# Kernel tuning notes

Measured on AMD Instinct MI355X. Metric: run time of the kernel, lower is better.

The kernel has to match this reference:

```python
import jax, jax.numpy as jnp
import numpy as np

B, C, OUT, H, W, M1, M2, HID = 4, 64, 64, 256, 256, 32, 32, 64
COORD = C + 1  # MLP input: channels + 1 coordinate


def _lin(key, fan_in, fan_out):
    lim = 1.0 / np.sqrt(fan_in)
    kw, kb = jax.random.split(key)
    Wm = jax.random.uniform(kw, (fan_in, fan_out), minval=-lim, maxval=lim, dtype=jnp.float32)
    b = jax.random.uniform(kb, (fan_out,), minval=-lim, maxval=lim, dtype=jnp.float32)
    return Wm, b


def setup_inputs() -> dict:
    key = jax.random.key(0)
    ks = jax.random.split(key, 12)
    x = jax.random.normal(ks[0], (B, C, H, W), dtype=jnp.float32)
    # basis_w MLP: (C+1) -> HID -> HID -> 2*M2
    wW0, wb0 = _lin(ks[1], COORD, HID)
    wW1, wb1 = _lin(ks[2], HID, HID)
    wW2, wb2 = _lin(ks[3], HID, 2 * M2)
    # basis_h MLP: (C+1) -> HID -> HID -> 2*M1
    hW0, hb0 = _lin(ks[4], COORD, HID)
    hW1, hb1 = _lin(ks[5], HID, HID)
    hW2, hb2 = _lin(ks[6], HID, 2 * M1)
    std = (1.0 / (C + OUT)) ** 0.5
    Wf_re = std * jax.random.normal(ks[7], (C, OUT, M1, M2), dtype=jnp.float32)
    Wf_im = std * jax.random.normal(ks[8], (C, OUT, M1, M2), dtype=jnp.float32)
    mixer_w, mixer_b = _lin(ks[9], OUT, OUT)
    mixer_w = mixer_w.T  # (out, in) conv1x1 layout
    sc_w, sc_b = _lin(ks[10], C, OUT)
    sc_w = sc_w.T
    return {
        "x": x,
        "wW0": wW0, "wb0": wb0, "wW1": wW1, "wb1": wb1, "wW2": wW2, "wb2": wb2,
        "hW0": hW0, "hb0": hb0, "hW1": hW1, "hb1": hb1, "hW2": hW2, "hb2": hb2,
        "Wf_re": Wf_re, "Wf_im": Wf_im,
        "mixer_w": mixer_w, "mixer_b": mixer_b,
        "sc_w": sc_w, "sc_b": sc_b,
    }


def _gelu(v):
    return jax.nn.gelu(v, approximate=False)  # torch GELU is exact erf


def _cmlp(x, W0, b0, W1, b1, W2, b2, m):
    h = _gelu(x @ W0 + b0)
    h = _gelu(h @ W1 + b1)
    o = h @ W2 + b2
    return jax.lax.complex(o[..., :m], o[..., m:])


def reference(x, wW0, wb0, wW1, wb1, wW2, wb2,
              hW0, hb0, hW1, hb1, hW2, hb2,
              Wf_re, Wf_im, mixer_w, mixer_b, sc_w, sc_b):
    Bb, Cc, Hh, Ww = x.shape
    # --- W-direction basis: input is (values, w-coord) per pixel ---
    wc = jnp.linspace(-1.0, 1.0, Ww, dtype=jnp.float32)
    w_in = jnp.concatenate(
        [jnp.transpose(x, (0, 2, 3, 1)),
         jnp.broadcast_to(wc[None, None, :, None], (Bb, Hh, Ww, 1))], axis=-1)
    wb = _cmlp(w_in, wW0, wb0, wW1, wb1, wW2, wb2, M2)  # (B,H,W,m2) complex
    xc = x.astype(jnp.complex64)
    # separable transform along W: contract W against runtime basis
    tfw = jnp.einsum('bchw,bhwm->bchm', xc, wb)  # (B,C,H,m2)
    # --- H-direction basis: input is real part of W-transform + h-coord ---
    hcv = jnp.linspace(-1.0, 1.0, Hh, dtype=jnp.float32)
    h_in = jnp.concatenate(
        [jnp.transpose(tfw.real, (0, 3, 2, 1)),
         jnp.broadcast_to(hcv[None, None, :, None], (Bb, M2, Hh, 1))], axis=-1)
    hb = _cmlp(h_in, hW0, hb0, hW1, hb1, hW2, hb2, M1)  # (B,m2,H,m1) complex
    tfhw = jnp.einsum('bchm,bmhk->bckm', tfw, hb)  # (B,C,m1,m2)
    Wf = jax.lax.complex(Wf_re, Wf_im)  # (C_in, C_out, m1, m2)
    proc = jnp.einsum('bixy,oixy->boxy', tfhw, Wf)  # (B,out,m1,m2)
    # inverse transforms with conjugate-transposed bases
    rec = jnp.einsum('bokm,bmhk->bohm', proc, jnp.conj(hb))  # (B,out,H,m2)
    spatial = jnp.einsum('bohm,bhwm->bohw', rec, jnp.conj(wb)).real / (Hh * Ww)
    y = jnp.einsum('bchw,oc->bohw', spatial, mixer_w) + mixer_b[None, :, None, None]
    y = _gelu(y)
    y = y + jnp.einsum('bchw,oc->bohw', x, sc_w) + sc_b[None, :, None, None]
    return _gelu(y)
```

## Files before the change

kernel.cpp:

```cpp
#include <hip/hip_runtime.h>
#include <math.h>


typedef __attribute__((ext_vector_type(8))) short bf16x8;
typedef __attribute__((ext_vector_type(4))) float f32x4;

__device__ __forceinline__ float gelu_f(float v) {
    const float u = v * 0.70710678118654752440f;
    const float xa = fabsf(u);
    const float t = __builtin_amdgcn_rcpf(fmaf(0.3275911f, xa, 1.0f));
    float p = fmaf(1.061405429f, t, -1.453152027f);
    p = fmaf(p, t, 1.421413741f);
    p = fmaf(p, t, -0.284496736f);
    p = fmaf(p, t, 0.254829592f);
    p *= t;
    const float e = __expf(-xa * xa);
    float erfv = fmaf(-p, e, 1.0f);
    erfv = (u < 0.0f) ? -erfv : erfv;
    return 0.5f * v * (1.0f + erfv);
}

__device__ __forceinline__ unsigned short f2b(float f) {
    union { float f; unsigned int u; } v; v.f = f;
    unsigned int u = v.u + 0x7FFFu + ((v.u >> 16) & 1u);
    return (unsigned short)(u >> 16);
}
__device__ __forceinline__ float b2f(unsigned short b) {
    union { unsigned int u; float f; } v; v.u = ((unsigned int)b) << 16;
    return v.f;
}

constexpr int MLD = 104;
constexpr int XLD = 72;

__device__ __forceinline__ ushort4 butterfly_xT(const float4 v, int q) {
    const float bx = __shfl_xor(v.x, 1);
    const float by = __shfl_xor(v.y, 1);
    const float bz = __shfl_xor(v.z, 1);
    const float bw = __shfl_xor(v.w, 1);
    float4 s1;
    s1.x = ((q & 1) == 0) ? v.x : by;
    s1.y = ((q & 1) == 0) ? bx  : v.y;
    s1.z = ((q & 1) == 0) ? v.z : bw;
    s1.w = ((q & 1) == 0) ? bz  : v.w;
    const float cx = __shfl_xor(s1.x, 2);
    const float cy = __shfl_xor(s1.y, 2);
    const float cz = __shfl_xor(s1.z, 2);
    const float cw = __shfl_xor(s1.w, 2);
    float4 s2;
    s2.x = ((q & 2) == 0) ? s1.x : cz;
    s2.y = ((q & 2) == 0) ? s1.y : cw;
    s2.z = ((q & 2) == 0) ? cx   : s1.z;
    s2.w = ((q & 2) == 0) ? cy   : s1.w;
    ushort4 u;
    u.x = f2b(s2.x); u.y = f2b(s2.y); u.z = f2b(s2.z); u.w = f2b(s2.w);
    return u;
}

__device__ __forceinline__ void stage_xT(const float* __restrict__ x,
    unsigned short* __restrict__ sA, int b, int h, int w0, int t, int LD)
{
    const int lane = t & 63, wv = t >> 6;
    const int q = lane & 3, wg = lane >> 2;
#pragma unroll
    for (int r = 0; r < 4; ++r) {
        const int cb = (r * 4 + wv) * 4;
        const float4 v = *(const float4*)&x[((size_t)(b * 64 + cb + q) * 256 + h) * 256 + w0 + wg * 4];
        const ushort4 u = butterfly_xT(v, q);
        *(ushort4*)&sA[(wg * 4 + q) * LD + cb] = u;
    }
}

__global__ void k_prep(const float* __restrict__ wW0, const float* __restrict__ wW1,
                       const float* __restrict__ wW2,
                       const float* __restrict__ hW0, const float* __restrict__ hW1,
                       const float* __restrict__ hW2,
                       unsigned short* __restrict__ wT0, unsigned short* __restrict__ wT1,
                       unsigned short* __restrict__ wT2,
                       unsigned short* __restrict__ hT0, unsigned short* __restrict__ hT1,
                       unsigned short* __restrict__ hT2)
{
    const int t = threadIdx.x;
    for (int idx = t; idx < 64 * 96; idx += 256) {
        const int o = idx / 96, k = idx % 96;
        wT0[idx] = (k < 65) ? f2b(wW0[k * 64 + o]) : (unsigned short)0;
        hT0[idx] = (k < 65) ? f2b(hW0[k * 64 + o]) : (unsigned short)0;
    }
    for (int idx = t; idx < 4096; idx += 256) {
        const int o = idx >> 6, k = idx & 63;
        wT1[idx] = f2b(wW1[k * 64 + o]);
        wT2[idx] = f2b(wW2[k * 64 + o]);
        hT1[idx] = f2b(hW1[k * 64 + o]);
        hT2[idx] = f2b(hW2[k * 64 + o]);
    }
}

__global__ __launch_bounds__(256) void k_psum(const float* __restrict__ src,
                                              float* __restrict__ dst,
                                              int nparts, int part_stride)
{
    const int i = (blockIdx.x * 256 + threadIdx.x) * 4;
    float4 acc = *(const float4*)&src[i];
    for (int p = 1; p < nparts; ++p) {
        const float4 v = *(const float4*)&src[(size_t)p * part_stride + i];
        acc.x += v.x; acc.y += v.y; acc.z += v.z; acc.w += v.w;
    }
    *(float4*)&dst[i] = acc;
}

__global__ __launch_bounds__(256) void k_psum_procT(const float* __restrict__ src,
                                                    float* __restrict__ dst)
{
    const int idx = blockIdx.x * 256 + threadIdx.x;
    const int o = idx & 63, k = (idx >> 6) & 31, m = (idx >> 11) & 31, b = idx >> 16;
    const size_t in = (size_t)(b * 64 + o) * 1024 + k * 32 + m;
    const float re = src[in] + src[524288 + in];
    const float im = src[262144 + in] + src[524288 + 262144 + in];
    dst[idx] = re;
    dst[262144 + idx] = im;
}

template<bool GELU, int NKC>
__device__ __forceinline__ void mfma_layer(
    const unsigned short* __restrict__ sW,
    const unsigned short* __restrict__ sAct,
    unsigned short* __restrict__ dst,
    const float* __restrict__ bias, int lane, int wv)
{
    const int arow = lane & 15;
    const int koff = (lane >> 4) * 8;
    const int crow = 16 * wv + (lane >> 4) * 4;
    const f32x4 zero = {0.f, 0.f, 0.f, 0.f};
    f32x4 acc[4] = {zero, zero, zero, zero};
#pragma unroll
    for (int kc = 0; kc < NKC; ++kc) {
        const bf16x8 a = *(const bf16x8*)&sW[(16 * wv + arow) * MLD + kc * 32 + koff];
#pragma unroll
        for (int nt = 0; nt < 4; ++nt) {
            const bf16x8 b = *(const bf16x8*)&sAct[(nt * 16 + arow) * MLD + kc * 32 + koff];
            acc[nt] = __builtin_amdgcn_mfma_f32_16x16x32_bf16(a, b, acc[nt], 0, 0, 0);
        }
    }
    const float4 bv = *(const float4*)&bias[crow];
#pragma unroll
    for (int nt = 0; nt < 4; ++nt) {
        const int px = nt * 16 + arow;
        float v0 = acc[nt][0] + bv.x;
        float v1 = acc[nt][1] + bv.y;
        float v2 = acc[nt][2] + bv.z;
        float v3 = acc[nt][3] + bv.w;
        if (GELU) { v0 = gelu_f(v0); v1 = gelu_f(v1); v2 = gelu_f(v2); v3 = gelu_f(v3); }
        ushort4 u;
        u.x = f2b(v0); u.y = f2b(v1); u.z = f2b(v2); u.w = f2b(v3);
        *(ushort4*)&dst[px * MLD + crow] = u;
    }
}

__device__ __forceinline__ void stage_wT96(const unsigned short* __restrict__ src,
                                           unsigned short* __restrict__ sW, int t) {
#pragma unroll
    for (int r = 0; r < 3; ++r) {
        const int idx = r * 256 + t;
        const int row = idx / 12, f = idx % 12;
        *(uint4*)&sW[row * MLD + f * 8] = *(const uint4*)&src[row * 96 + f * 8];
    }
}
__device__ __forceinline__ void stage_wT64(const unsigned short* __restrict__ src,
                                           unsigned short* __restrict__ sW, int t) {
#pragma unroll
    for (int r = 0; r < 2; ++r) {
        const int idx = r * 256 + t;
        const int row = idx >> 3, f = idx & 7;
        *(uint4*)&sW[row * MLD + f * 8] = *(const uint4*)&src[row * 64 + f * 8];
    }
}

template<bool GELU, int NKC>
__device__ __forceinline__ void mfma_layer_s(
    const unsigned short* __restrict__ sW,
    const unsigned short* __restrict__ sAct,
    unsigned short* __restrict__ dst,
    const float* __restrict__ bias, int lane, int wv)
{
    const int arow = lane & 15;
    const int g = lane >> 4;
    const int crow = 16 * wv + g * 4;
    const int sx7 = arow & 7, sx3 = arow & 3;
    const f32x4 zero = {0.f, 0.f, 0.f, 0.f};
    f32x4 acc[4] = {zero, zero, zero, zero};
#pragma unroll
    for (int kc = 0; kc < NKC; ++kc) {
        const int chraw = kc * 4 + g;
        const int ch = (chraw < 8) ? (chraw ^ sx7) : (8 + ((chraw - 8) ^ sx3));
        const bf16x8 a = *(const bf16x8*)&sW[(16 * wv + arow) * 96 + ch * 8];
#pragma unroll
        for (int nt = 0; nt < 4; ++nt) {
            const bf16x8 b = *(const bf16x8*)&sAct[(nt * 16 + arow) * 96 + ch * 8];
            acc[nt] = __builtin_amdgcn_mfma_f32_16x16x32_bf16(a, b, acc[nt], 0, 0, 0);
        }
    }
    const float4 bv = *(const float4*)&bias[crow];
    const int chw = (crow >> 3) ^ sx7;
#pragma unroll
    for (int nt = 0; nt < 4; ++nt) {
        const int px = nt * 16 + arow;
        float v0 = acc[nt][0] + bv.x;
        float v1 = acc[nt][1] + bv.y;
        float v2 = acc[nt][2] + bv.z;
        float v3 = acc[nt][3] + bv.w;
        if (GELU) { v0 = gelu_f(v0); v1 = gelu_f(v1); v2 = gelu_f(v2); v3 = gelu_f(v3); }
        ushort4 u;
        u.x = f2b(v0); u.y = f2b(v1); u.z = f2b(v2); u.w = f2b(v3);
        *(ushort4*)&dst[px * 96 + chw * 8 + (crow & 7)] = u;
    }
}

__device__ __forceinline__ void stage_wT96_s(const unsigned short* __restrict__ src,
                                             unsigned short* __restrict__ sW, int t) {
#pragma unroll
    for (int r = 0; r < 3; ++r) {
        const int idx = r * 256 + t;
        const int row = idx / 12, f = idx % 12;
        const int ch = (f < 8) ? (f ^ (row & 7)) : (8 + ((f - 8) ^ (row & 3)));
        *(uint4*)&sW[row * 96 + ch * 8] = *(const uint4*)&src[row * 96 + f * 8];
    }
}
__device__ __forceinline__ void stage_wT64_s(const unsigned short* __restrict__ src,
                                             unsigned short* __restrict__ sW, int t) {
#pragma unroll
    for (int r = 0; r < 2; ++r) {
        const int idx = r * 256 + t;
        const int row = idx >> 3, f = idx & 7;
        *(uint4*)&sW[row * 96 + ((f ^ (row & 7)) << 3)] = *(const uint4*)&src[row * 64 + f * 8];
    }
}

__global__ __launch_bounds__(256) void k_wbtfw(
    const float* __restrict__ x,
    const unsigned short* __restrict__ wT0, const float* __restrict__ b0,
    const unsigned short* __restrict__ wT1, const float* __restrict__ b1,
    const unsigned short* __restrict__ wT2, const float* __restrict__ b2,
    unsigned short* __restrict__ wb_bf, float* __restrict__ tfwM)
{
    __shared__ __align__(16) unsigned short smem[26624];
    unsigned short* sA   = smem;
    unsigned short* sB   = smem + 6144;
    unsigned short* sW   = smem + 12288;
    unsigned short* sXt  = smem + 18432;
    unsigned short* sWBt = smem + 22528;

    const int bh = blockIdx.x;
    const int b = bh >> 8, h = bh & 255;
    const int t = threadIdx.x;
    const int lane = t & 63, wv = t >> 6;
    const int arow = lane & 15, g = lane >> 4;
    const int crow = 16 * wv + g * 4;
    const int sx7 = arow & 7;
    const f32x4 zero = {0.f, 0.f, 0.f, 0.f};

    f32x4 atf[4] = {zero, zero, zero, zero};

    for (int wq = 0; wq < 4; ++wq) {
        const int w0 = wq * 64;
        __syncthreads();
        {
            const int q = lane & 3, wg = lane >> 2;
#pragma unroll
            for (int r = 0; r < 4; ++r) {
                const int cb = 16 * r + 4 * wv;
                const int c = cb + q;
                const float4 v = *(const float4*)&x[((size_t)(b * 64 + c) * 256 + h) * 256 + w0 + wg * 4];
                ushort4 ux;
                ux.x = f2b(v.x); ux.y = f2b(v.y); ux.z = f2b(v.z); ux.w = f2b(v.w);
                const int chx = (wg >> 1) ^ (c & 7);
                *(ushort4*)&sXt[c * 64 + chx * 8 + 4 * (wg & 1)] = ux;
                const ushort4 u = butterfly_xT(v, q);
                const int row = wg * 4 + q;
                const int cha = (cb >> 3) ^ (row & 7);
                *(ushort4*)&sA[row * 96 + cha * 8 + (cb & 7)] = u;
            }
        }
        if (t < 64) {
            const uint4 z = {0, 0, 0, 0};
#pragma unroll
            for (int j = 0; j < 4; ++j)
                *(uint4*)&sA[t * 96 + (8 + (j ^ (t & 3))) * 8] = z;
            sA[t * 96 + (8 + (t & 3)) * 8] = f2b((float)(w0 + t) * (2.0f / 255.0f) - 1.0f);
        }
        stage_wT96_s(wT0, sW, t);
        __syncthreads();
        mfma_layer_s<true, 3>(sW, sA, sB, b0, lane, wv);
        __syncthreads();
        stage_wT64_s(wT1, sW, t);
        __syncthreads();
        mfma_layer_s<true, 2>(sW, sB, sA, b1, lane, wv);
        __syncthreads();
        stage_wT64_s(wT2, sW, t);
        __syncthreads();
        {
            f32x4 acc[4] = {zero, zero, zero, zero};
#pragma unroll
            for (int kc = 0; kc < 2; ++kc) {
                const int ch = (kc * 4 + g) ^ sx7;
                const bf16x8 a = *(const bf16x8*)&sW[(16 * wv + arow) * 96 + ch * 8];
#pragma unroll
                for (int nt = 0; nt < 4; ++nt) {
                    const bf16x8 bb = *(const bf16x8*)&sA[(nt * 16 + arow) * 96 + ch * 8];
                    acc[nt] = __builtin_amdgcn_mfma_f32_16x16x32_bf16(a, bb, acc[nt], 0, 0, 0);
                }
            }
            const float4 bv = *(const float4*)&b2[crow];
            const int chw = (crow >> 3) ^ sx7;
#pragma unroll
            for (int nt = 0; nt < 4; ++nt) {
                const int px = nt * 16 + arow;
                ushort4 u;
                u.x = f2b(acc[nt][0] + bv.x);
                u.y = f2b(acc[nt][1] + bv.y);
                u.z = f2b(acc[nt][2] + bv.z);
                u.w = f2b(acc[nt][3] + bv.w);
                *(ushort4*)&sB[px * 96 + chw * 8 + (crow & 7)] = u;
                const int ph = px >> 3, pl = px & 7;
                sWBt[(crow + 0) * 64 + ((ph ^ ((crow + 0) & 7)) << 3) + pl] = u.x;
                sWBt[(crow + 1) * 64 + ((ph ^ ((crow + 1) & 7)) << 3) + pl] = u.y;
                sWBt[(crow + 2) * 64 + ((ph ^ ((crow + 2) & 7)) << 3) + pl] = u.z;
                sWBt[(crow + 3) * 64 + ((ph ^ ((crow + 3) & 7)) << 3) + pl] = u.w;
            }
        }
        __syncthreads();
        const size_t pixbase = (size_t)(b * 256 + h) * 256 + w0;
#pragma unroll
        for (int r = 0; r < 2; ++r) {
            const int idx = r * 256 + t;
            const int px = idx >> 3, f = idx & 7;
            *(uint4*)&wb_bf[(pixbase + px) * 64 + f * 8] =
                *(const uint4*)&sB[px * 96 + ((f ^ (px & 7)) << 3)];
        }
#pragma unroll
        for (int kc = 0; kc < 2; ++kc) {
            const int ch = (kc * 4 + g) ^ sx7;
            const bf16x8 a = *(const bf16x8*)&sWBt[(16 * wv + arow) * 64 + ch * 8];
#pragma unroll
            for (int nt = 0; nt < 4; ++nt) {
                const bf16x8 bb = *(const bf16x8*)&sXt[(nt * 16 + arow) * 64 + ch * 8];
                atf[nt] = __builtin_amdgcn_mfma_f32_16x16x32_bf16(a, bb, atf[nt], 0, 0, 0);
            }
        }
    }

    __syncthreads();
    float* sF = (float*)smem;
#pragma unroll
    for (int nt = 0; nt < 4; ++nt) {
        const int c = nt * 16 + arow;
#pragma unroll
        for (int j = 0; j < 4; ++j)
            sF[(crow + j) * 68 + c] = atf[nt][j];
    }
    __syncthreads();
#pragma unroll
    for (int r = 0; r < 4; ++r) {
        const int idx = r * 256 + t;
        const int m = idx >> 5, gg = idx & 31;
        float4 v;
        v.x = sF[m * 68 + gg * 2];
        v.y = sF[(m + 32) * 68 + gg * 2];
        v.z = sF[m * 68 + gg * 2 + 1];
        v.w = sF[(m + 32) * 68 + gg * 2 + 1];
        *(float4*)&tfwM[((size_t)(b * 32 + m) * 256 + h) * 128 + gg * 4] = v;
    }
}

__global__ __launch_bounds__(256) void k_hb_mlp2(
    const float* __restrict__ tfwM,
    const unsigned short* __restrict__ hT0, const float* __restrict__ b0,
    const unsigned short* __restrict__ hT1, const float* __restrict__ b1,
    const unsigned short* __restrict__ hT2, const float* __restrict__ b2,
    unsigned short* __restrict__ hb_bf)
{
    __shared__ __align__(16) unsigned short sA[64 * MLD];
    __shared__ __align__(16) unsigned short sB[64 * MLD];
    __shared__ __align__(16) unsigned short sW[65 * MLD];
    const int blk = blockIdx.x;
    const int bm = blk >> 2, hq = blk & 3;
    const int h0 = hq * 64;
    const int t = threadIdx.x;
    const int lane = t & 63, wv = t >> 6;

#pragma unroll
    for (int r = 0; r < 4; ++r) {
        const int idx = r * 256 + t;
        const int p = idx >> 4, f = idx & 15;
        const float* src = &tfwM[(size_t)(bm * 256 + h0 + p) * 128 + f * 8];
        const float4 u0 = *(const float4*)&src[0];
        const float4 u1 = *(const float4*)&src[4];
        ushort4 u;
        u.x = f2b(u0.x); u.y = f2b(u0.z); u.z = f2b(u1.x); u.w = f2b(u1.z);
        *(ushort4*)&sA[p * MLD + f * 4] = u;
    }
    if (t < 64) {
        const uint4 z = {0, 0, 0, 0};
        *(uint4*)&sA[t * MLD + 64] = z;
        *(uint4*)&sA[t * MLD + 72] = z;
        *(uint4*)&sA[t * MLD + 80] = z;
        *(uint4*)&sA[t * MLD + 88] = z;
        sA[t * MLD + 64] = f2b((float)(h0 + t) * (2.0f / 255.0f) - 1.0f);
    }
    stage_wT96(hT0, sW, t);
    __syncthreads();
    mfma_layer<true, 3>(sW, sA, sB, b0, lane, wv);
    __syncthreads();
    stage_wT64(hT1, sW, t);
    __syncthreads();
    mfma_layer<true, 2>(sW, sB, sA, b1, lane, wv);
    __syncthreads();
    stage_wT64(hT2, sW, t);
    __syncthreads();
    mfma_layer<false, 2>(sW, sA, sB, b2, lane, wv);
    __syncthreads();

    const size_t pixbase = (size_t)bm * 256 + h0;
#pragma unroll
    for (int r = 0; r < 2; ++r) {
        const int idx = r * 256 + t;
        const int px = idx >> 3, f = idx & 7;
        *(uint4*)&hb_bf[(pixbase + px) * 64 + f * 8] = *(const uint4*)&sB[px * MLD + f * 8];
    }
}

__global__ __launch_bounds__(256) void k_tfhw3(
    const float* __restrict__ tfwM,
    const unsigned short* __restrict__ hb_bf,
    float* __restrict__ tfhw_p)
{
    __shared__ float hr[64 * 32];
    __shared__ float hi2[64 * 32];
    __shared__ float slab[32 * 64];
    const int blk = blockIdx.x;
    const int bm = blk >> 3, chalf = (blk >> 2) & 1, hq = blk & 3;
    const int b = bm >> 5, m = bm & 31;
    const int t = threadIdx.x;
#pragma unroll
    for (int r = 0; r < 2; ++r) {
        const int q = r * 256 + t;
        const int hl = q >> 3, f = q & 7;
        const uint4 raw = *(const uint4*)&hb_bf[((size_t)bm * 256 + hq * 64 + hl) * 64 + f * 8];
        const unsigned short* us = (const unsigned short*)&raw;
        float v[8];
#pragma unroll
        for (int j = 0; j < 8; ++j) v[j] = b2f(us[j]);
        float* dst = (f < 4) ? &hr[hl * 32 + f * 8] : &hi2[hl * 32 + (f - 4) * 8];
        float4 lo; lo.x = v[0]; lo.y = v[1]; lo.z = v[2]; lo.w = v[3];
        float4 hi; hi.x = v[4]; hi.y = v[5]; hi.z = v[6]; hi.w = v[7];
        *(float4*)&dst[0] = lo;
        *(float4*)&dst[4] = hi;
    }
    const int k = t & 31, cq = t >> 5;
    float accr[4] = {0.f, 0.f, 0.f, 0.f}, acci[4] = {0.f, 0.f, 0.f, 0.f};
    const size_t tbase = (size_t)bm * 32768;
    for (int ht = 0; ht < 2; ++ht) {
        __syncthreads();
#pragma unroll
        for (int r = 0; r < 2; ++r) {
            const int q = r * 256 + t;
            const int hl = q >> 3, f = q & 7;
            *(float4*)&slab[hl * 64 + f * 4] =
                *(const float4*)&tfwM[tbase + (size_t)(hq * 64 + ht * 32 + hl) * 128 + chalf * 64 + f * 4];
        }
        __syncthreads();
#pragma unroll 8
        for (int hl = 0; hl < 32; ++hl) {
            const float hrv = hr[(ht * 32 + hl) * 32 + k];
            const float hiv = hi2[(ht * 32 + hl) * 32 + k];
            const float4 u0 = *(const float4*)&slab[hl * 64 + cq * 8];
            const float4 u1 = *(const float4*)&slab[hl * 64 + cq * 8 + 4];
            accr[0] = fmaf(u0.x, hrv, fmaf(-u0.y, hiv, accr[0]));
            acci[0] = fmaf(u0.x, hiv, fmaf( u0.y, hrv, acci[0]));
            accr[1] = fmaf(u0.z, hrv, fmaf(-u0.w, hiv, accr[1]));
            acci[1] = fmaf(u0.z, hiv, fmaf( u0.w, hrv, acci[1]));
            accr[2] = fmaf(u1.x, hrv, fmaf(-u1.y, hiv, accr[2]));
            acci[2] = fmaf(u1.x, hiv, fmaf( u1.y, hrv, acci[2]));
            accr[3] = fmaf(u1.z, hrv, fmaf(-u1.w, hiv, accr[3]));
            acci[3] = fmaf(u1.z, hiv, fmaf( u1.w, hrv, acci[3]));
        }
    }
    float* tp = tfhw_p + (size_t)hq * 524288;
#pragma unroll
    for (int i = 0; i < 4; ++i) {
        const int c = chalf * 32 + cq * 4 + i;
        const size_t po = ((size_t)(b * 64 + c) * 32 + k) * 32 + m;
        tp[po] = accr[i];
        tp[262144 + po] = acci[i];
    }
}

__global__ __launch_bounds__(256) void k_proc2(
    const float* __restrict__ tfhw,
    const float* __restrict__ Wf_re, const float* __restrict__ Wf_im,
    float* __restrict__ proc_p)
{
    const int blk = blockIdx.x;
    const int o = blk >> 3, kq = (blk >> 1) & 3, chalf = blk & 1;
    const int t = threadIdx.x;
    const int mo = kq * 256 + t;
    const float* tre = tfhw;
    const float* tim = tfhw + 262144;
    float accr[4] = {0.f, 0.f, 0.f, 0.f}, acci[4] = {0.f, 0.f, 0.f, 0.f};
    for (int cc = 0; cc < 32; ++cc) {
        const int c = chalf * 32 + cc;
        const float wfr = Wf_re[(size_t)(c * 64 + o) * 1024 + mo];
        const float wfi = Wf_im[(size_t)(c * 64 + o) * 1024 + mo];
#pragma unroll
        for (int bb = 0; bb < 4; ++bb) {
            const float tr = tre[(size_t)(bb * 64 + c) * 1024 + mo];
            const float ti = tim[(size_t)(bb * 64 + c) * 1024 + mo];
            accr[bb] = fmaf(tr, wfr, fmaf(-ti, wfi, accr[bb]));
            acci[bb] = fmaf(tr, wfi, fmaf(ti, wfr, acci[bb]));
        }
    }
    float* pp = proc_p + (size_t)chalf * 524288;
#pragma unroll
    for (int bb = 0; bb < 4; ++bb) {
        pp[(size_t)(bb * 64 + o) * 1024 + mo] = accr[bb];
        pp[262144 + (size_t)(bb * 64 + o) * 1024 + mo] = acci[bb];
    }
}

__global__ __launch_bounds__(256) void k_rec4(
    const float* __restrict__ procT,
    const unsigned short* __restrict__ hb_bf,
    unsigned short* __restrict__ recO)
{
    __shared__ float lhr[32 * 32];
    __shared__ float lhi[32 * 32];
    const int blk = blockIdx.x;
    const int bm = blk >> 3, hq = blk & 7;
    const int b = bm >> 5, m = bm & 31;
    const int t = threadIdx.x;
    {
        const int hl = t >> 3, f = t & 7;
        const uint4 raw = *(const uint4*)&hb_bf[((size_t)bm * 256 + hq * 32 + hl) * 64 + f * 8];
        const unsigned short* us = (const unsigned short*)&raw;
        float v[8];
#pragma unroll
        for (int j = 0; j < 8; ++j) v[j] = b2f(us[j]);
        float* dst = (f < 4) ? &lhr[hl * 32 + f * 8] : &lhi[hl * 32 + (f - 4) * 8];
        float4 lo; lo.x = v[0]; lo.y = v[1]; lo.z = v[2]; lo.w = v[3];
        float4 hi; hi.x = v[4]; hi.y = v[5]; hi.z = v[6]; hi.w = v[7];
        *(float4*)&dst[0] = lo;
        *(float4*)&dst[4] = hi;
    }
    const int o = t & 63, hg = t >> 6;
    const float* pr = procT + (size_t)(b * 32 + m) * 2048 + o;
    const float* pi = pr + 262144;
    float Pr[32], Pi[32];
#pragma unroll
    for (int k = 0; k < 32; ++k) {
        Pr[k] = pr[k * 64];
        Pi[k] = pi[k * 64];
    }
    __syncthreads();
    for (int hh = 0; hh < 8; ++hh) {
        const int hl = hg * 8 + hh;
        float ar = 0.f, ai = 0.f;
#pragma unroll
        for (int k4 = 0; k4 < 8; ++k4) {
            const float4 hr4 = *(const float4*)&lhr[hl * 32 + k4 * 4];
            const float4 hi4 = *(const float4*)&lhi[hl * 32 + k4 * 4];
            ar = fmaf(Pr[k4*4+0], hr4.x, fmaf(Pi[k4*4+0], hi4.x, ar));
            ai = fmaf(Pi[k4*4+0], hr4.x, fmaf(-Pr[k4*4+0], hi4.x, ai));
            ar = fmaf(Pr[k4*4+1], hr4.y, fmaf(Pi[k4*4+1], hi4.y, ar));
            ai = fmaf(Pi[k4*4+1], hr4.y, fmaf(-Pr[k4*4+1], hi4.y, ai));
            ar = fmaf(Pr[k4*4+2], hr4.z, fmaf(Pi[k4*4+2], hi4.z, ar));
            ai = fmaf(Pi[k4*4+2], hr4.z, fmaf(-Pr[k4*4+2], hi4.z, ai));
            ar = fmaf(Pr[k4*4+3], hr4.w, fmaf(Pi[k4*4+3], hi4.w, ar));
            ai = fmaf(Pi[k4*4+3], hr4.w, fmaf(-Pr[k4*4+3], hi4.w, ai));
        }
        const int h = hq * 32 + hl;
        const size_t rb = ((size_t)(b * 256 + h) * 64 + o) * 64;
        recO[rb + m]      = f2b(ar);
        recO[rb + 32 + m] = f2b(ai);
    }
}

__global__ __launch_bounds__(256) void k_final4(
    const float* __restrict__ x,
    const unsigned short* __restrict__ wb_bf,
    const unsigned short* __restrict__ recO,
    const float* __restrict__ mw, const float* __restrict__ mb,
    const float* __restrict__ scw, const float* __restrict__ scb,
    float* __restrict__ out)
{
    constexpr int LD = 72;
    __shared__ __align__(16) unsigned short sWb[64 * LD];
    __shared__ __align__(16) unsigned short sR [64 * LD];
    __shared__ __align__(16) unsigned short sX [64 * LD];
    __shared__ __align__(16) unsigned short sS [64 * LD];
    const int blk = blockIdx.x;
    const int b = blk >> 10, h = (blk >> 2) & 255, wq = blk & 3;
    const int w0 = wq * 64;
    const int t = threadIdx.x;
    const int lane = t & 63, wv = t >> 6;
    const size_t pixbase = (size_t)(b * 256 + h) * 256 + w0;

#pragma unroll
    for (int r = 0; r < 2; ++r) {
        const int idx = r * 256 + t;
        const int px = idx >> 3, f = idx & 7;
        *(uint4*)&sWb[px * LD + f * 8] = *(const uint4*)&wb_bf[(pixbase + px) * 64 + f * 8];
    }
    const size_t recbase = (size_t)(b * 256 + h) * 4096;
#pragma unroll
    for (int r = 0; r < 2; ++r) {
        const int idx = r * 256 + t;
        const int o = idx >> 3, f = idx & 7;
        *(uint4*)&sR[o * LD + f * 8] = *(const uint4*)&recO[recbase + (size_t)o * 64 + f * 8];
    }
    stage_xT(x, sX, b, h, w0, t, LD);
    __syncthreads();

    const int arow = lane & 15;
    const int koff = (lane >> 4) * 8;
    const f32x4 zero = {0.f, 0.f, 0.f, 0.f};

    f32x4 accA[4] = {zero, zero, zero, zero};
#pragma unroll
    for (int kc = 0; kc < 2; ++kc) {
        const bf16x8 a = *(const bf16x8*)&sR[(16 * wv + arow) * LD + kc * 32 + koff];
#pragma unroll
        for (int nt = 0; nt < 4; ++nt) {
            const bf16x8 bb = *(const bf16x8*)&sWb[(nt * 16 + arow) * LD + kc * 32 + koff];
            accA[nt] = __builtin_amdgcn_mfma_f32_16x16x32_bf16(a, bb, accA[nt], 0, 0, 0);
        }
    }
    __syncthreads();

    const int crow = 16 * wv + (lane >> 4) * 4;
#pragma unroll
    for (int nt = 0; nt < 4; ++nt) {
        const int px = nt * 16 + arow;
#pragma unroll
        for (int j = 0; j < 4; ++j)
            sS[px * LD + crow + j] = f2b(accA[nt][j] * (1.0f / 65536.0f));
    }
#pragma unroll
    for (int r = 0; r < 4; ++r) {
        const int idx = r * 256 + t;
        const int o = idx >> 4, cq = idx & 15;
        const float4 v1 = *(const float4*)&mw[o * 64 + cq * 4];
        ushort4 u1;
        u1.x = f2b(v1.x); u1.y = f2b(v1.y); u1.z = f2b(v1.z); u1.w = f2b(v1.w);
        *(ushort4*)&sWb[o * LD + cq * 4] = u1;
        const float4 v2 = *(const float4*)&scw[o * 64 + cq * 4];
        ushort4 u2;
        u2.x = f2b(v2.x); u2.y = f2b(v2.y); u2.z = f2b(v2.z); u2.w = f2b(v2.w);
        *(ushort4*)&sR[o * LD + cq * 4] = u2;
    }
    __syncthreads();

    f32x4 accB[4] = {zero, zero, zero, zero};
    f32x4 accC[4] = {zero, zero, zero, zero};
#pragma unroll
    for (int kc = 0; kc < 2; ++kc) {
        const bf16x8 am = *(const bf16x8*)&sWb[(16 * wv + arow) * LD + kc * 32 + koff];
        const bf16x8 as = *(const bf16x8*)&sR [(16 * wv + arow) * LD + kc * 32 + koff];
#pragma unroll
        for (int nt = 0; nt < 4; ++nt) {
            const bf16x8 bs = *(const bf16x8*)&sS[(nt * 16 + arow) * LD + kc * 32 + koff];
            const bf16x8 bx = *(const bf16x8*)&sX[(nt * 16 + arow) * LD + kc * 32 + koff];
            accB[nt] = __builtin_amdgcn_mfma_f32_16x16x32_bf16(am, bs, accB[nt], 0, 0, 0);
            accC[nt] = __builtin_amdgcn_mfma_f32_16x16x32_bf16(as, bx, accC[nt], 0, 0, 0);
        }
    }

#pragma unroll
    for (int nt = 0; nt < 4; ++nt) {
        const int px = nt * 16 + arow;
#pragma unroll
        for (int j = 0; j < 4; ++j) {
            const int o = crow + j;
            const float y = gelu_f(accB[nt][j] + mb[o]);
            const float z = y + accC[nt][j] + scb[o];
            out[((size_t)(b * 64 + o) * 256 + h) * 256 + w0 + px] = gelu_f(z);
        }
    }
}

extern "C" void kernel_launch(void* const* d_in, const int* in_sizes, int n_in,
                              void* d_out, int out_size, void* d_ws, size_t ws_size,
                              hipStream_t stream) {
    const float* x    = (const float*)d_in[0];
    const float* wW0  = (const float*)d_in[1];
    const float* wb0  = (const float*)d_in[2];
    const float* wW1  = (const float*)d_in[3];
    const float* wb1  = (const float*)d_in[4];
    const float* wW2  = (const float*)d_in[5];
    const float* wb2  = (const float*)d_in[6];
    const float* hW0  = (const float*)d_in[7];
    const float* hb0  = (const float*)d_in[8];
    const float* hW1  = (const float*)d_in[9];
    const float* hb1  = (const float*)d_in[10];
    const float* hW2  = (const float*)d_in[11];
    const float* hb2  = (const float*)d_in[12];
    const float* Wf_re = (const float*)d_in[13];
    const float* Wf_im = (const float*)d_in[14];
    const float* mw   = (const float*)d_in[15];
    const float* mbv  = (const float*)d_in[16];
    const float* scw  = (const float*)d_in[17];
    const float* scb  = (const float*)d_in[18];

    char* base = (char*)d_ws;
    unsigned short* wb_bf = (unsigned short*)(base + 0);
    float* tfwM   = (float*)(base + 33554432);
    unsigned short* hb_bf = (unsigned short*)(base + 50331648);
    float* tfhw_p = (float*)(base + 54525952);
    float* tfhw   = (float*)(base + 62914560);
    float* proc_p = (float*)(base + 65011712);
    float* procT  = (float*)(base + 69206016);
    unsigned short* recO = (unsigned short*)(base + 71303168);
    unsigned short* wT0 = (unsigned short*)(base + 79691776);
    unsigned short* wT1 = (unsigned short*)(base + 79704064);
    unsigned short* wT2 = (unsigned short*)(base + 79712256);
    unsigned short* hT0 = (unsigned short*)(base + 79720448);
    unsigned short* hT1 = (unsigned short*)(base + 79732736);
    unsigned short* hT2 = (unsigned short*)(base + 79740928);

    k_prep<<<1, 256, 0, stream>>>(wW0, wW1, wW2, hW0, hW1, hW2,
                                  wT0, wT1, wT2, hT0, hT1, hT2);
    k_wbtfw<<<1024, 256, 0, stream>>>(x, wT0, wb0, wT1, wb1, wT2, wb2, wb_bf, tfwM);
    k_hb_mlp2<<<512, 256, 0, stream>>>(tfwM, hT0, hb0, hT1, hb1, hT2, hb2, hb_bf);
    k_tfhw3<<<1024, 256, 0, stream>>>(tfwM, hb_bf, tfhw_p);
    k_psum<<<1024, 256, 0, stream>>>(tfhw_p, tfhw, 4, 524288);
    k_proc2<<<512, 256, 0, stream>>>(tfhw, Wf_re, Wf_im, proc_p);
    k_psum_procT<<<1024, 256, 0, stream>>>(proc_p, procT);
    k_rec4<<<1024, 256, 0, stream>>>(procT, hb_bf, recO);
    k_final4<<<4096, 256, 0, stream>>>(x, wb_bf, recO, mw, mbv, scw, scb, (float*)d_out);
}
```

Before: 184.7 us.

## Hold MLP weights in registers and reuse bf16 transposed x in final kernel

The MLP weight fragments and biases are now loaded straight into registers once per block, in both the W-basis and H-basis MLP kernels. This removes the repeated shared-memory weight staging and the barriers between layers. The W-basis kernel also writes the bf16 transposed x tile it already builds to a new workspace buffer. The final kernel then loads that buffer instead of re-reading fp32 x and shuffling it into transposed form. The H-MLP moves to the swizzled 96-wide shared layout. The cost is more registers, an extra 32MB write, and a larger workspace.

```diff
diff --git a/kernel.cpp b/kernel.cpp
--- a/kernel.cpp
+++ b/kernel.cpp
@@ -29,9 +29,6 @@
     union { unsigned int u; float f; } v; v.u = ((unsigned int)b) << 16;
     return v.f;
 }
-
-constexpr int MLD = 104;
-constexpr int XLD = 72;
 
 __device__ __forceinline__ ushort4 butterfly_xT(const float4 v, int q) {
     const float bx = __shfl_xor(v.x, 1);
@@ -57,20 +54,6 @@
     return u;
 }
 
-__device__ __forceinline__ void stage_xT(const float* __restrict__ x,
-    unsigned short* __restrict__ sA, int b, int h, int w0, int t, int LD)
-{
-    const int lane = t & 63, wv = t >> 6;
-    const int q = lane & 3, wg = lane >> 2;
-#pragma unroll
-    for (int r = 0; r < 4; ++r) {
-        const int cb = (r * 4 + wv) * 4;
-        const float4 v = *(const float4*)&x[((size_t)(b * 64 + cb + q) * 256 + h) * 256 + w0 + wg * 4];
-        const ushort4 u = butterfly_xT(v, q);
-        *(ushort4*)&sA[(wg * 4 + q) * LD + cb] = u;
-    }
-}
-
 __global__ void k_prep(const float* __restrict__ wW0, const float* __restrict__ wW1,
                        const float* __restrict__ wW2,
                        const float* __restrict__ hW0, const float* __restrict__ hW1,
@@ -121,69 +104,12 @@
 }
 
 template<bool GELU, int NKC>
-__device__ __forceinline__ void mfma_layer(
-    const unsigned short* __restrict__ sW,
+__device__ __forceinline__ void mfma_layer_r(
+    const bf16x8* __restrict__ wf,
     const unsigned short* __restrict__ sAct,
     unsigned short* __restrict__ dst,
-    const float* __restrict__ bias, int lane, int wv)
-{
-    const int arow = lane & 15;
-    const int koff = (lane >> 4) * 8;
-    const int crow = 16 * wv + (lane >> 4) * 4;
-    const f32x4 zero = {0.f, 0.f, 0.f, 0.f};
-    f32x4 acc[4] = {zero, zero, zero, zero};
-#pragma unroll
-    for (int kc = 0; kc < NKC; ++kc) {
-        const bf16x8 a = *(const bf16x8*)&sW[(16 * wv + arow) * MLD + kc * 32 + koff];
-#pragma unroll
-        for (int nt = 0; nt < 4; ++nt) {
-            const bf16x8 b = *(const bf16x8*)&sAct[(nt * 16 + arow) * MLD + kc * 32 + koff];
-            acc[nt] = __builtin_amdgcn_mfma_f32_16x16x32_bf16(a, b, acc[nt], 0, 0, 0);
-        }
-    }
-    const float4 bv = *(const float4*)&bias[crow];
-#pragma unroll
-    for (int nt = 0; nt < 4; ++nt) {
-        const int px = nt * 16 + arow;
-        float v0 = acc[nt][0] + bv.x;
-        float v1 = acc[nt][1] + bv.y;
-        float v2 = acc[nt][2] + bv.z;
-        float v3 = acc[nt][3] + bv.w;
-        if (GELU) { v0 = gelu_f(v0); v1 = gelu_f(v1); v2 = gelu_f(v2); v3 = gelu_f(v3); }
-        ushort4 u;
-        u.x = f2b(v0); u.y = f2b(v1); u.z = f2b(v2); u.w = f2b(v3);
-        *(ushort4*)&dst[px * MLD + crow] = u;
-    }
-}
-
-__device__ __forceinline__ void stage_wT96(const unsigned short* __restrict__ src,
-                                           unsigned short* __restrict__ sW, int t) {
-#pragma unroll
-    for (int r = 0; r < 3; ++r) {
-        const int idx = r * 256 + t;
-        const int row = idx / 12, f = idx % 12;
-        *(uint4*)&sW[row * MLD + f * 8] = *(const uint4*)&src[row * 96 + f * 8];
-    }
-}
-__device__ __forceinline__ void stage_wT64(const unsigned short* __restrict__ src,
-                                           unsigned short* __restrict__ sW, int t) {
-#pragma unroll
-    for (int r = 0; r < 2; ++r) {
-        const int idx = r * 256 + t;
-        const int row = idx >> 3, f = idx & 7;
-        *(uint4*)&sW[row * MLD + f * 8] = *(const uint4*)&src[row * 64 + f * 8];
-    }
-}
-
-template<bool GELU, int NKC>
-__device__ __forceinline__ void mfma_layer_s(
-    const unsigned short* __restrict__ sW,
-    const unsigned short* __restrict__ sAct,
-    unsigned short* __restrict__ dst,
-    const float* __restrict__ bias, int lane, int wv)
-{
-    const int arow = lane & 15;
-    const int g = lane >> 4;
+    const float4 bv, int arow, int g, int wv)
+{
     const int crow = 16 * wv + g * 4;
     const int sx7 = arow & 7, sx3 = arow & 3;
     const f32x4 zero = {0.f, 0.f, 0.f, 0.f};
@@ -192,14 +118,12 @@
     for (int kc = 0; kc < NKC; ++kc) {
         const int chraw = kc * 4 + g;
         const int ch = (chraw < 8) ? (chraw ^ sx7) : (8 + ((chraw - 8) ^ sx3));
-        const bf16x8 a = *(const bf16x8*)&sW[(16 * wv + arow) * 96 + ch * 8];
 #pragma unroll
         for (int nt = 0; nt < 4; ++nt) {
             const bf16x8 b = *(const bf16x8*)&sAct[(nt * 16 + arow) * 96 + ch * 8];
-            acc[nt] = __builtin_amdgcn_mfma_f32_16x16x32_bf16(a, b, acc[nt], 0, 0, 0);
-        }
-    }
-    const float4 bv = *(const float4*)&bias[crow];
+            acc[nt] = __builtin_amdgcn_mfma_f32_16x16x32_bf16(wf[kc], b, acc[nt], 0, 0, 0);
+        }
+    }
     const int chw = (crow >> 3) ^ sx7;
 #pragma unroll
     for (int nt = 0; nt < 4; ++nt) {
@@ -215,39 +139,19 @@
     }
 }
 
-__device__ __forceinline__ void stage_wT96_s(const unsigned short* __restrict__ src,
-                                             unsigned short* __restrict__ sW, int t) {
-#pragma unroll
-    for (int r = 0; r < 3; ++r) {
-        const int idx = r * 256 + t;
-        const int row = idx / 12, f = idx % 12;
-        const int ch = (f < 8) ? (f ^ (row & 7)) : (8 + ((f - 8) ^ (row & 3)));
-        *(uint4*)&sW[row * 96 + ch * 8] = *(const uint4*)&src[row * 96 + f * 8];
-    }
-}
-__device__ __forceinline__ void stage_wT64_s(const unsigned short* __restrict__ src,
-                                             unsigned short* __restrict__ sW, int t) {
-#pragma unroll
-    for (int r = 0; r < 2; ++r) {
-        const int idx = r * 256 + t;
-        const int row = idx >> 3, f = idx & 7;
-        *(uint4*)&sW[row * 96 + ((f ^ (row & 7)) << 3)] = *(const uint4*)&src[row * 64 + f * 8];
-    }
-}
-
 __global__ __launch_bounds__(256) void k_wbtfw(
     const float* __restrict__ x,
     const unsigned short* __restrict__ wT0, const float* __restrict__ b0,
     const unsigned short* __restrict__ wT1, const float* __restrict__ b1,
     const unsigned short* __restrict__ wT2, const float* __restrict__ b2,
-    unsigned short* __restrict__ wb_bf, float* __restrict__ tfwM)
-{
-    __shared__ __align__(16) unsigned short smem[26624];
+    unsigned short* __restrict__ wb_bf, unsigned short* __restrict__ xT_bf,
+    float* __restrict__ tfwM)
+{
+    __shared__ __align__(16) unsigned short smem[20480];
     unsigned short* sA   = smem;
     unsigned short* sB   = smem + 6144;
-    unsigned short* sW   = smem + 12288;
-    unsigned short* sXt  = smem + 18432;
-    unsigned short* sWBt = smem + 22528;
+    unsigned short* sXt  = smem + 12288;
+    unsigned short* sWBt = smem + 16384;
 
     const int bh = blockIdx.x;
     const int b = bh >> 8, h = bh & 255;
@@ -257,6 +161,20 @@
     const int crow = 16 * wv + g * 4;
     const int sx7 = arow & 7;
     const f32x4 zero = {0.f, 0.f, 0.f, 0.f};
+
+    const int wrow = 16 * wv + arow;
+    bf16x8 w0f[3], w1f[2], w2f[2];
+#pragma unroll
+    for (int kc = 0; kc < 3; ++kc)
+        w0f[kc] = *(const bf16x8*)&wT0[wrow * 96 + (kc * 4 + g) * 8];
+#pragma unroll
+    for (int kc = 0; kc < 2; ++kc) {
+        w1f[kc] = *(const bf16x8*)&wT1[wrow * 64 + (kc * 4 + g) * 8];
+        w2f[kc] = *(const bf16x8*)&wT2[wrow * 64 + (kc * 4 + g) * 8];
+    }
+    const float4 bv0 = *(const float4*)&b0[crow];
+    const float4 bv1 = *(const float4*)&b1[crow];
+    const float4 bv2 = *(const float4*)&b2[crow];
 
     f32x4 atf[4] = {zero, zero, zero, zero};
 
@@ -287,38 +205,39 @@
                 *(uint4*)&sA[t * 96 + (8 + (j ^ (t & 3))) * 8] = z;
             sA[t * 96 + (8 + (t & 3)) * 8] = f2b((float)(w0 + t) * (2.0f / 255.0f) - 1.0f);
         }
-        stage_wT96_s(wT0, sW, t);
         __syncthreads();
-        mfma_layer_s<true, 3>(sW, sA, sB, b0, lane, wv);
+        const size_t pixbase = (size_t)(b * 256 + h) * 256 + w0;
+#pragma unroll
+        for (int r = 0; r < 2; ++r) {
+            const int idx = r * 256 + t;
+            const int px = idx >> 3, f = idx & 7;
+            *(uint4*)&xT_bf[(pixbase + px) * 64 + f * 8] =
+                *(const uint4*)&sA[px * 96 + ((f ^ (px & 7)) << 3)];
+        }
+        mfma_layer_r<true, 3>(w0f, sA, sB, bv0, arow, g, wv);
         __syncthreads();
-        stage_wT64_s(wT1, sW, t);
-        __syncthreads();
-        mfma_layer_s<true, 2>(sW, sB, sA, b1, lane, wv);
-        __syncthreads();
-        stage_wT64_s(wT2, sW, t);
+        mfma_layer_r<true, 2>(w1f, sB, sA, bv1, arow, g, wv);
         __syncthreads();
         {
             f32x4 acc[4] = {zero, zero, zero, zero};
 #pragma unroll
             for (int kc = 0; kc < 2; ++kc) {
                 const int ch = (kc * 4 + g) ^ sx7;
-                const bf16x8 a = *(const bf16x8*)&sW[(16 * wv + arow) * 96 + ch * 8];
 #pragma unroll
                 for (int nt = 0; nt < 4; ++nt) {
                     const bf16x8 bb = *(const bf16x8*)&sA[(nt * 16 + arow) * 96 + ch * 8];
-                    acc[nt] = __builtin_amdgcn_mfma_f32_16x16x32_bf16(a, bb, acc[nt], 0, 0, 0);
+                    acc[nt] = __builtin_amdgcn_mfma_f32_16x16x32_bf16(w2f[kc], bb, acc[nt], 0, 0, 0);
                 }
             }
-            const float4 bv = *(const float4*)&b2[crow];
             const int chw = (crow >> 3) ^ sx7;
 #pragma unroll
             for (int nt = 0; nt < 4; ++nt) {
                 const int px = nt * 16 + arow;
                 ushort4 u;
-                u.x = f2b(acc[nt][0] + bv.x);
-                u.y = f2b(acc[nt][1] + bv.y);
-                u.z = f2b(acc[nt][2] + bv.z);
-                u.w = f2b(acc[nt][3] + bv.w);
+                u.x = f2b(acc[nt][0] + bv2.x);
+                u.y = f2b(acc[nt][1] + bv2.y);
+                u.z = f2b(acc[nt][2] + bv2.z);
+                u.w = f2b(acc[nt][3] + bv2.w);
                 *(ushort4*)&sB[px * 96 + chw * 8 + (crow & 7)] = u;
                 const int ph = px >> 3, pl = px & 7;
                 sWBt[(crow + 0) * 64 + ((ph ^ ((crow + 0) & 7)) << 3) + pl] = u.x;
@@ -328,7 +247,6 @@
             }
         }
         __syncthreads();
-        const size_t pixbase = (size_t)(b * 256 + h) * 256 + w0;
 #pragma unroll
         for (int r = 0; r < 2; ++r) {
             const int idx = r * 256 + t;
@@ -371,21 +289,36 @@
     }
 }
 
-__global__ __launch_bounds__(256) void k_hb_mlp2(
+__global__ __launch_bounds__(256) void k_hb_mlp3(
     const float* __restrict__ tfwM,
     const unsigned short* __restrict__ hT0, const float* __restrict__ b0,
     const unsigned short* __restrict__ hT1, const float* __restrict__ b1,
     const unsigned short* __restrict__ hT2, const float* __restrict__ b2,
     unsigned short* __restrict__ hb_bf)
 {
-    __shared__ __align__(16) unsigned short sA[64 * MLD];
-    __shared__ __align__(16) unsigned short sB[64 * MLD];
-    __shared__ __align__(16) unsigned short sW[65 * MLD];
+    __shared__ __align__(16) unsigned short sA[64 * 96];
+    __shared__ __align__(16) unsigned short sB[64 * 96];
     const int blk = blockIdx.x;
     const int bm = blk >> 2, hq = blk & 3;
     const int h0 = hq * 64;
     const int t = threadIdx.x;
     const int lane = t & 63, wv = t >> 6;
+    const int arow = lane & 15, g = lane >> 4;
+    const int crow = 16 * wv + g * 4;
+
+    const int wrow = 16 * wv + arow;
+    bf16x8 h0f[3], h1f[2], h2f[2];
+#pragma unroll
+    for (int kc = 0; kc < 3; ++kc)
+        h0f[kc] = *(const bf16x8*)&hT0[wrow * 96 + (kc * 4 + g) * 8];
+#pragma unroll
+    for (int kc = 0; kc < 2; ++kc) {
+        h1f[kc] = *(const bf16x8*)&hT1[wrow * 64 + (kc * 4 + g) * 8];
+        h2f[kc] = *(const bf16x8*)&hT2[wrow * 64 + (kc * 4 + g) * 8];
+    }
+    const float4 bv0 = *(const float4*)&b0[crow];
+    const float4 bv1 = *(const float4*)&b1[crow];
+    const float4 bv2 = *(const float4*)&b2[crow];
 
 #pragma unroll
     for (int r = 0; r < 4; ++r) {
@@ -396,27 +329,22 @@
         const float4 u1 = *(const float4*)&src[4];
         ushort4 u;
         u.x = f2b(u0.x); u.y = f2b(u0.z); u.z = f2b(u1.x); u.w = f2b(u1.z);
-        *(ushort4*)&sA[p * MLD + f * 4] = u;
+        const int ch = (f >> 1) ^ (p & 7);
+        *(ushort4*)&sA[p * 96 + ch * 8 + 4 * (f & 1)] = u;
     }
     if (t < 64) {
         const uint4 z = {0, 0, 0, 0};
-        *(uint4*)&sA[t * MLD + 64] = z;
-        *(uint4*)&sA[t * MLD + 72] = z;
-        *(uint4*)&sA[t * MLD + 80] = z;
-        *(uint4*)&sA[t * MLD + 88] = z;
-        sA[t * MLD + 64] = f2b((float)(h0 + t) * (2.0f / 255.0f) - 1.0f);
-    }
-    stage_wT96(hT0, sW, t);
-    __syncthreads();
-    mfma_layer<true, 3>(sW, sA, sB, b0, lane, wv);
-    __syncthreads();
-    stage_wT64(hT1, sW, t);
-    __syncthreads();
-    mfma_layer<true, 2>(sW, sB, sA, b1, lane, wv);
-    __syncthreads();
-    stage_wT64(hT2, sW, t);
-    __syncthreads();
-    mfma_layer<false, 2>(sW, sA, sB, b2, lane, wv);
+#pragma unroll
+        for (int j = 0; j < 4; ++j)
+            *(uint4*)&sA[t * 96 + (8 + (j ^ (t & 3))) * 8] = z;
+        sA[t * 96 + (8 + (t & 3)) * 8] = f2b((float)(h0 + t) * (2.0f / 255.0f) - 1.0f);
+    }
+    __syncthreads();
+    mfma_layer_r<true, 3>(h0f, sA, sB, bv0, arow, g, wv);
+    __syncthreads();
+    mfma_layer_r<true, 2>(h1f, sB, sA, bv1, arow, g, wv);
+    __syncthreads();
+    mfma_layer_r<false, 2>(h2f, sA, sB, bv2, arow, g, wv);
     __syncthreads();
 
     const size_t pixbase = (size_t)bm * 256 + h0;
@@ -424,7 +352,8 @@
     for (int r = 0; r < 2; ++r) {
         const int idx = r * 256 + t;
         const int px = idx >> 3, f = idx & 7;
-        *(uint4*)&hb_bf[(pixbase + px) * 64 + f * 8] = *(const uint4*)&sB[px * MLD + f * 8];
+        *(uint4*)&hb_bf[(pixbase + px) * 64 + f * 8] =
+            *(const uint4*)&sB[px * 96 + ((f ^ (px & 7)) << 3)];
     }
 }
 
@@ -584,7 +513,7 @@
 }
 
 __global__ __launch_bounds__(256) void k_final4(
-    const float* __restrict__ x,
+    const unsigned short* __restrict__ xT_bf,
     const unsigned short* __restrict__ wb_bf,
     const unsigned short* __restrict__ recO,
     const float* __restrict__ mw, const float* __restrict__ mb,
@@ -616,7 +545,12 @@
         const int o = idx >> 3, f = idx & 7;
         *(uint4*)&sR[o * LD + f * 8] = *(const uint4*)&recO[recbase + (size_t)o * 64 + f * 8];
     }
-    stage_xT(x, sX, b, h, w0, t, LD);
+#pragma unroll
+    for (int r = 0; r < 2; ++r) {
+        const int idx = r * 256 + t;
+        const int px = idx >> 3, f = idx & 7;
+        *(uint4*)&sX[px * LD + f * 8] = *(const uint4*)&xT_bf[(pixbase + px) * 64 + f * 8];
+    }
     __syncthreads();
 
     const int arow = lane & 15;
@@ -711,28 +645,31 @@
 
     char* base = (char*)d_ws;
     unsigned short* wb_bf = (unsigned short*)(base + 0);
-    float* tfwM   = (float*)(base + 33554432);
-    unsigned short* hb_bf = (unsigned short*)(base + 50331648);
-    float* tfhw_p = (float*)(base + 54525952);
-    float* tfhw   = (float*)(base + 62914560);
-    float* proc_p = (float*)(base + 65011712);
-    float* procT  = (float*)(base + 69206016);
-    unsigned short* recO = (unsigned short*)(base + 71303168);
-    unsigned short* wT0 = (unsigned short*)(base + 79691776);
-    unsigned short* wT1 = (unsigned short*)(base + 79704064);
-    unsigned short* wT2 = (unsigned short*)(base + 79712256);
-    unsigned short* hT0 = (unsigned short*)(base + 79720448);
-    unsigned short* hT1 = (unsigned short*)(base + 79732736);
-    unsigned short* hT2 = (unsigned short*)(base + 79740928);
+    unsigned short* xT_bf = (unsigned short*)(base + 33554432);
+    float* tfwM   = (float*)(base + 67108864);
+    unsigned short* hb_bf = (unsigned short*)(base + 83886080);
+    float* tfhw_p = (float*)(base + 88080384);
+    float* tfhw   = (float*)(base + 96468992);
+    float* proc_p = (float*)(base + 98566144);
+    float* procT  = (float*)(base + 102760448);
+    unsigned short* recO = (unsigned short*)(base + 104857600);
+    unsigned short* wT0 = (unsigned short*)(base + 113246208);
+    unsigned short* wT1 = (unsigned short*)(base + 113258496);
+    unsigned short* wT2 = (unsigned short*)(base + 113266688);
+    unsigned short* hT0 = (unsigned short*)(base + 113274880);
+    unsigned short* hT1 = (unsigned short*)(base + 113287168);
+    unsigned short* hT2 = (unsigned short*)(base + 113295360);
 
     k_prep<<<1, 256, 0, stream>>>(wW0, wW1, wW2, hW0, hW1, hW2,
                                   wT0, wT1, wT2, hT0, hT1, hT2);
-    k_wbtfw<<<1024, 256, 0, stream>>>(x, wT0, wb0, wT1, wb1, wT2, wb2, wb_bf, tfwM);
-    k_hb_mlp2<<<512, 256, 0, stream>>>(tfwM, hT0, hb0, hT1, hb1, hT2, hb2, hb_bf);
+    k_wbtfw<<<1024, 256, 0, stream>>>(x, wT0, wb0, wT1, wb1, wT2, wb2,
+                                      wb_bf, xT_bf, tfwM);
+    k_hb_mlp3<<<512, 256, 0, stream>>>(tfwM, hT0, hb0, hT1, hb1, hT2, hb2, hb_bf);
     k_tfhw3<<<1024, 256, 0, stream>>>(tfwM, hb_bf, tfhw_p);
     k_psum<<<1024, 256, 0, stream>>>(tfhw_p, tfhw, 4, 524288);
     k_proc2<<<512, 256, 0, stream>>>(tfhw, Wf_re, Wf_im, proc_p);
     k_psum_procT<<<1024, 256, 0, stream>>>(proc_p, procT);
     k_rec4<<<1024, 256, 0, stream>>>(procT, hb_bf, recO);
-    k_final4<<<4096, 256, 0, stream>>>(x, wb_bf, recO, mw, mbv, scw, scb, (float*)d_out);
-}
+    k_final4<<<4096, 256, 0, stream>>>(xT_bf, wb_bf, recO, mw, mbv, scw, scb,
+                                       (float*)d_out);
+}
```

After: 193.2 us. 1.05x slower.
